# Kernel optimization log

Measured on AMD Instinct MI355X. Metric: run time of the kernel, lower is better.

Reference implementation:

```python
import jax, jax.numpy as jnp
import numpy as np

B = 4096          # batch of users
HIST = 200        # interacted items per user (padded/fixed)
NNEG = 20         # negatives per user
M_ITEM = 100000
DIM = 64
ALPHA = 0.5
BATA = 1e-4
LAMDA = 1e-4


def setup_inputs() -> dict:
    key = jax.random.key(0)
    k1, k2, k3, k4, k5, k6 = jax.random.split(key, 6)
    pos_items = jax.random.randint(k1, (B,), 0, M_ITEM)
    neg_items = jax.random.randint(k2, (B, NNEG), 0, M_ITEM)
    interacted_items = jax.random.randint(k3, (B, HIST), 0, M_ITEM)
    # per-user interaction counts (positive floats; original does num ** -alpha)
    user_item_num = jax.random.randint(k4, (B,), 1, 201).astype(jnp.float32)
    pu = jax.random.normal(k5, (M_ITEM, DIM), dtype=jnp.float32) * 0.001
    qi = jax.random.normal(k6, (M_ITEM, DIM), dtype=jnp.float32) * 0.001
    bi = jnp.zeros((M_ITEM, 1), dtype=jnp.float32)
    return {
        "pos_items": pos_items,
        "neg_items": neg_items,
        "user_item_num": user_item_num,
        "interacted_items": interacted_items,
        "pu": pu,
        "qi": qi,
        "bi": bi,
    }


def reference(pos_items, neg_items, user_item_num, interacted_items, pu, qi, bi):
    # EmbeddingBag-style ragged gather-sum: user embedding = sum of pu rows
    # of the user's interacted items. [B, HIST, DIM] -> [B, DIM]
    user_embeds = jnp.sum(pu[interacted_items], axis=1)

    b_i_i = bi[pos_items]            # [B, 1]
    b_i_j = bi[neg_items]            # [B, NNEG, 1]
    pos_embeds = qi[pos_items]       # [B, DIM]
    neg_embeds = qi[neg_items]       # [B, NNEG, DIM]

    t = user_item_num ** (-ALPHA)    # [B]

    # diag(user @ pos^T) == rowwise dot product
    pos_scores = t * jnp.sum(user_embeds * pos_embeds, axis=1) + b_i_i.T          # [1, B]
    neg_dot = jnp.einsum("bd,bnd->bn", user_embeds, neg_embeds)                    # [B, NNEG]
    neg_scores = t * neg_dot.T + b_i_j[:, :, 0].T                                  # [NNEG, B]

    # MSELoss(reduction='sum')(ones, pos - neg)
    diff = 1.0 - (pos_scores - neg_scores)                                         # [NNEG, B]
    loss = jnp.sum(diff ** 2)
    loss = loss \
        + BATA * jnp.sum(user_embeds ** 2) \
        + BATA * (jnp.sum(pos_embeds ** 2) + jnp.sum(neg_embeds ** 2)) \
        + LAMDA * (jnp.sum(b_i_i ** 2) + jnp.sum(b_i_j ** 2))
    return loss
```

## Files before the change

### kernel.cpp

```cpp
#include <hip/hip_runtime.h>

#define NB 4096
#define HIST 200
#define NNEG 20
#define DIM 64
#define BATA 1e-4f
#define LAMDA 1e-4f

__global__ __launch_bounds__(256) void fism_kernel(
    const int* __restrict__ pos_items,
    const int* __restrict__ neg_items,
    const float* __restrict__ user_item_num,
    const int* __restrict__ interacted,
    const float* __restrict__ pu,
    const float* __restrict__ qi,
    const float* __restrict__ bi,
    float* __restrict__ partials)
{
    const int wave = threadIdx.x >> 6;
    const int lane = threadIdx.x & 63;
    const int g    = lane >> 4;
    const int c    = lane & 15;
    const int gid  = wave * 4 + g;
    const int b    = blockIdx.x;

    __shared__ float4 s_u[4][16];
    __shared__ float  s_dot[24];
    __shared__ float  s_qsq[24];

    const float4* pu4 = (const float4*)pu;
    const float4* qi4 = (const float4*)qi;
    const int*    it  = interacted + b * HIST;
    const int*    negp = neg_items + b * NNEG;

    const int posi = pos_items[b];

    const int4* it4 = (const int4*)(it + gid * 12);
    int4 i0 = it4[0], i1 = it4[1], i2 = it4[2];
    int  tidx = it[192 + (gid & 7)];

    const int item0 = (gid == 0) ? posi : negp[gid - 1];
    float4 q0 = qi4[item0 * (DIM / 4) + c];
    float4 q1 = make_float4(0.f, 0.f, 0.f, 0.f);
    if (gid < 5) {
        int item1 = negp[gid + 15];
        q1 = qi4[item1 * (DIM / 4) + c];
    }

    float t_pow = 0.f, bp = 0.f, bn = 0.f;
    if (wave == 0) {
        t_pow = user_item_num[b];
        bp = bi[posi];
        if (lane < NNEG) bn = bi[negp[lane]];
    }

    float4 a0 = make_float4(0.f, 0.f, 0.f, 0.f);
    float4 a1 = make_float4(0.f, 0.f, 0.f, 0.f);
    {
        float4 v0  = pu4[i0.x * (DIM / 4) + c];
        float4 v1  = pu4[i0.y * (DIM / 4) + c];
        float4 v2  = pu4[i0.z * (DIM / 4) + c];
        float4 v3  = pu4[i0.w * (DIM / 4) + c];
        float4 v4  = pu4[i1.x * (DIM / 4) + c];
        float4 v5  = pu4[i1.y * (DIM / 4) + c];
        float4 v6  = pu4[i1.z * (DIM / 4) + c];
        float4 v7  = pu4[i1.w * (DIM / 4) + c];
        float4 v8  = pu4[i2.x * (DIM / 4) + c];
        float4 v9  = pu4[i2.y * (DIM / 4) + c];
        float4 v10 = pu4[i2.z * (DIM / 4) + c];
        float4 v11 = pu4[i2.w * (DIM / 4) + c];
        float4 vt  = pu4[tidx * (DIM / 4) + c];

        a0.x += v0.x + v1.x; a0.y += v0.y + v1.y; a0.z += v0.z + v1.z; a0.w += v0.w + v1.w;
        a1.x += v2.x + v3.x; a1.y += v2.y + v3.y; a1.z += v2.z + v3.z; a1.w += v2.w + v3.w;
        a0.x += v4.x + v5.x; a0.y += v4.y + v5.y; a0.z += v4.z + v5.z; a0.w += v4.w + v5.w;
        a1.x += v6.x + v7.x; a1.y += v6.y + v7.y; a1.z += v6.z + v7.z; a1.w += v6.w + v7.w;
        a0.x += v8.x + v9.x; a0.y += v8.y + v9.y; a0.z += v8.z + v9.z; a0.w += v8.w + v9.w;
        a1.x += v10.x + v11.x; a1.y += v10.y + v11.y; a1.z += v10.z + v11.z; a1.w += v10.w + v11.w;
        if (gid < 8) {
            a0.x += vt.x; a0.y += vt.y; a0.z += vt.z; a0.w += vt.w;
        }
    }
    float4 u = make_float4(a0.x + a1.x, a0.y + a1.y, a0.z + a1.z, a0.w + a1.w);

    #pragma unroll
    for (int m = 16; m <= 32; m <<= 1) {
        u.x += __shfl_xor(u.x, m);
        u.y += __shfl_xor(u.y, m);
        u.z += __shfl_xor(u.z, m);
        u.w += __shfl_xor(u.w, m);
    }
    if (lane < 16) s_u[wave][lane] = u;
    __syncthreads();

    float4 u0 = s_u[0][c], u1 = s_u[1][c], u2 = s_u[2][c], u3 = s_u[3][c];
    float4 ut = make_float4(u0.x + u1.x + u2.x + u3.x,
                            u0.y + u1.y + u2.y + u3.y,
                            u0.z + u1.z + u2.z + u3.z,
                            u0.w + u1.w + u2.w + u3.w);

    float contrib = 0.f;
    if (wave == 0 && g == 0)
        contrib += BATA * (ut.x*ut.x + ut.y*ut.y + ut.z*ut.z + ut.w*ut.w);

    {
        float dp = ut.x*q0.x + ut.y*q0.y + ut.z*q0.z + ut.w*q0.w;
        float qs = q0.x*q0.x + q0.y*q0.y + q0.z*q0.z + q0.w*q0.w;
        #pragma unroll
        for (int m = 1; m <= 8; m <<= 1) {
            dp += __shfl_xor(dp, m);
            qs += __shfl_xor(qs, m);
        }
        if (c == 0) { s_dot[gid] = dp; s_qsq[gid] = qs; }
    }
    if (gid < 5) {
        float dp = ut.x*q1.x + ut.y*q1.y + ut.z*q1.z + ut.w*q1.w;
        float qs = q1.x*q1.x + q1.y*q1.y + q1.z*q1.z + q1.w*q1.w;
        #pragma unroll
        for (int m = 1; m <= 8; m <<= 1) {
            dp += __shfl_xor(dp, m);
            qs += __shfl_xor(qs, m);
        }
        if (c == 0) { s_dot[gid + 16] = dp; s_qsq[gid + 16] = qs; }
    }
    __syncthreads();

    if (wave == 0) {
        const float t = 1.0f / sqrtf(t_pow);
        const float pos_score = t * s_dot[0] + bp;

        if (lane < NNEG) {
            float neg_score = t * s_dot[lane + 1] + bn;
            float d = 1.0f - pos_score + neg_score;
            contrib += d * d + LAMDA * bn * bn + BATA * s_qsq[lane + 1];
        }
        if (lane == 0)
            contrib += LAMDA * bp * bp + BATA * s_qsq[0];

        #pragma unroll
        for (int m = 1; m < 64; m <<= 1)
            contrib += __shfl_xor(contrib, m);
        if (lane == 0)
            partials[b] = contrib;
    }
}

__global__ __launch_bounds__(1024) void reduce_kernel(
    const float* __restrict__ part, float* __restrict__ out)
{
    __shared__ float s[16];
    const int t = threadIdx.x;
    float v = 0.f;
    #pragma unroll
    for (int k = 0; k < NB / 1024; ++k)
        v += part[t + k * 1024];
    #pragma unroll
    for (int m = 1; m < 64; m <<= 1)
        v += __shfl_xor(v, m);
    if ((t & 63) == 0) s[t >> 6] = v;
    __syncthreads();
    if (t < 16) {
        float x = s[t];
        #pragma unroll
        for (int m = 1; m < 16; m <<= 1)
            x += __shfl_xor(x, m);
        if (t == 0) out[0] = x;
    }
}

extern "C" void kernel_launch(void* const* d_in, const int* in_sizes, int n_in,
                              void* d_out, int out_size, void* d_ws, size_t ws_size,
                              hipStream_t stream) {
    const int*   pos_items     = (const int*)  d_in[0];
    const int*   neg_items     = (const int*)  d_in[1];
    const float* user_item_num = (const float*)d_in[2];
    const int*   interacted    = (const int*)  d_in[3];
    const float* pu            = (const float*)d_in[4];
    const float* qi            = (const float*)d_in[5];
    const float* bi            = (const float*)d_in[6];
    float* partials = (float*)d_ws;
    float* out = (float*)d_out;

    fism_kernel<<<NB, 256, 0, stream>>>(
        pos_items, neg_items, user_item_num, interacted, pu, qi, bi, partials);
    reduce_kernel<<<1, 1024, 0, stream>>>(partials, out);
}
```

Measured before the change: 38.48 us.

## Process eight users per block and reduce via atomicAdd instead of second kernel

Each block now loops over eight users, accumulating its loss locally and adding it to the output with a single atomicAdd. The output is zeroed with a memset, replacing the separate reduction kernel. This aims to cut per-block overhead and the second kernel launch. In exchange the grid shrinks, leaving fewer memory gathers in flight per CU, and users within a block are processed serially with barriers between them. Float atomics also make the summation order nondeterministic.

```diff
diff --git a/kernel.cpp b/kernel.cpp
--- a/kernel.cpp
+++ b/kernel.cpp
@@ -1,6 +1,8 @@
 #include <hip/hip_runtime.h>
 
 #define NB 4096
+#define UPB 8
+#define NBLK (NB / UPB)
 #define HIST 200
 #define NNEG 20
 #define DIM 64
@@ -15,14 +17,13 @@
     const float* __restrict__ pu,
     const float* __restrict__ qi,
     const float* __restrict__ bi,
-    float* __restrict__ partials)
+    float* __restrict__ out)
 {
     const int wave = threadIdx.x >> 6;
     const int lane = threadIdx.x & 63;
     const int g    = lane >> 4;
     const int c    = lane & 15;
     const int gid  = wave * 4 + g;
-    const int b    = blockIdx.x;
 
     __shared__ float4 s_u[4][16];
     __shared__ float  s_dot[24];
@@ -30,142 +31,127 @@
 
     const float4* pu4 = (const float4*)pu;
     const float4* qi4 = (const float4*)qi;
-    const int*    it  = interacted + b * HIST;
-    const int*    negp = neg_items + b * NNEG;
 
-    const int posi = pos_items[b];
+    float blockAcc = 0.f;
 
-    const int4* it4 = (const int4*)(it + gid * 12);
-    int4 i0 = it4[0], i1 = it4[1], i2 = it4[2];
-    int  tidx = it[192 + (gid & 7)];
+    for (int uu = 0; uu < UPB; ++uu) {
+        const int b = blockIdx.x * UPB + uu;
+        const int* it   = interacted + b * HIST;
+        const int* negp = neg_items + b * NNEG;
 
-    const int item0 = (gid == 0) ? posi : negp[gid - 1];
-    float4 q0 = qi4[item0 * (DIM / 4) + c];
-    float4 q1 = make_float4(0.f, 0.f, 0.f, 0.f);
-    if (gid < 5) {
-        int item1 = negp[gid + 15];
-        q1 = qi4[item1 * (DIM / 4) + c];
+        const int posi = pos_items[b];
+
+        const int4* it4 = (const int4*)(it + gid * 12);
+        int4 i0 = it4[0], i1 = it4[1], i2 = it4[2];
+        int  tidx = it[192 + (gid & 7)];
+
+        const int item0 = (gid == 0) ? posi : negp[gid - 1];
+        float4 q0 = qi4[item0 * (DIM / 4) + c];
+        float4 q1 = make_float4(0.f, 0.f, 0.f, 0.f);
+        if (gid < 5) {
+            int item1 = negp[gid + 15];
+            q1 = qi4[item1 * (DIM / 4) + c];
+        }
+
+        float t_pow = 0.f, bp = 0.f, bn = 0.f;
+        if (wave == 0) {
+            t_pow = user_item_num[b];
+            bp = bi[posi];
+            if (lane < NNEG) bn = bi[negp[lane]];
+        }
+
+        float4 a0 = make_float4(0.f, 0.f, 0.f, 0.f);
+        float4 a1 = make_float4(0.f, 0.f, 0.f, 0.f);
+        {
+            float4 v0  = pu4[i0.x * (DIM / 4) + c];
+            float4 v1  = pu4[i0.y * (DIM / 4) + c];
+            float4 v2  = pu4[i0.z * (DIM / 4) + c];
+            float4 v3  = pu4[i0.w * (DIM / 4) + c];
+            float4 v4  = pu4[i1.x * (DIM / 4) + c];
+            float4 v5  = pu4[i1.y * (DIM / 4) + c];
+            float4 v6  = pu4[i1.z * (DIM / 4) + c];
+            float4 v7  = pu4[i1.w * (DIM / 4) + c];
+            float4 v8  = pu4[i2.x * (DIM / 4) + c];
+            float4 v9  = pu4[i2.y * (DIM / 4) + c];
+            float4 v10 = pu4[i2.z * (DIM / 4) + c];
+            float4 v11 = pu4[i2.w * (DIM / 4) + c];
+            float4 vt  = pu4[tidx * (DIM / 4) + c];
+
+            a0.x += v0.x + v1.x; a0.y += v0.y + v1.y; a0.z += v0.z + v1.z; a0.w += v0.w + v1.w;
+            a1.x += v2.x + v3.x; a1.y += v2.y + v3.y; a1.z += v2.z + v3.z; a1.w += v2.w + v3.w;
+            a0.x += v4.x + v5.x; a0.y += v4.y + v5.y; a0.z += v4.z + v5.z; a0.w += v4.w + v5.w;
+            a1.x += v6.x + v7.x; a1.y += v6.y + v7.y; a1.z += v6.z + v7.z; a1.w += v6.w + v7.w;
+            a0.x += v8.x + v9.x; a0.y += v8.y + v9.y; a0.z += v8.z + v9.z; a0.w += v8.w + v9.w;
+            a1.x += v10.x + v11.x; a1.y += v10.y + v11.y; a1.z += v10.z + v11.z; a1.w += v10.w + v11.w;
+            if (gid < 8) {
+                a0.x += vt.x; a0.y += vt.y; a0.z += vt.z; a0.w += vt.w;
+            }
+        }
+        float4 u = make_float4(a0.x + a1.x, a0.y + a1.y, a0.z + a1.z, a0.w + a1.w);
+
+        #pragma unroll
+        for (int m = 16; m <= 32; m <<= 1) {
+            u.x += __shfl_xor(u.x, m);
+            u.y += __shfl_xor(u.y, m);
+            u.z += __shfl_xor(u.z, m);
+            u.w += __shfl_xor(u.w, m);
+        }
+        if (lane < 16) s_u[wave][lane] = u;
+        __syncthreads();
+
+        float4 u0 = s_u[0][c], u1 = s_u[1][c], u2 = s_u[2][c], u3 = s_u[3][c];
+        float4 ut = make_float4(u0.x + u1.x + u2.x + u3.x,
+                                u0.y + u1.y + u2.y + u3.y,
+                                u0.z + u1.z + u2.z + u3.z,
+                                u0.w + u1.w + u2.w + u3.w);
+
+        float contrib = 0.f;
+        if (wave == 0 && g == 0)
+            contrib += BATA * (ut.x*ut.x + ut.y*ut.y + ut.z*ut.z + ut.w*ut.w);
+
+        {
+            float dp = ut.x*q0.x + ut.y*q0.y + ut.z*q0.z + ut.w*q0.w;
+            float qs = q0.x*q0.x + q0.y*q0.y + q0.z*q0.z + q0.w*q0.w;
+            #pragma unroll
+            for (int m = 1; m <= 8; m <<= 1) {
+                dp += __shfl_xor(dp, m);
+                qs += __shfl_xor(qs, m);
+            }
+            if (c == 0) { s_dot[gid] = dp; s_qsq[gid] = qs; }
+        }
+        if (gid < 5) {
+            float dp = ut.x*q1.x + ut.y*q1.y + ut.z*q1.z + ut.w*q1.w;
+            float qs = q1.x*q1.x + q1.y*q1.y + q1.z*q1.z + q1.w*q1.w;
+            #pragma unroll
+            for (int m = 1; m <= 8; m <<= 1) {
+                dp += __shfl_xor(dp, m);
+                qs += __shfl_xor(qs, m);
+            }
+            if (c == 0) { s_dot[gid + 16] = dp; s_qsq[gid + 16] = qs; }
+        }
+        __syncthreads();
+
+        if (wave == 0) {
+            const float t = 1.0f / sqrtf(t_pow);
+            const float pos_score = t * s_dot[0] + bp;
+
+            if (lane < NNEG) {
+                float neg_score = t * s_dot[lane + 1] + bn;
+                float d = 1.0f - pos_score + neg_score;
+                contrib += d * d + LAMDA * bn * bn + BATA * s_qsq[lane + 1];
+            }
+            if (lane == 0)
+                contrib += LAMDA * bp * bp + BATA * s_qsq[0];
+
+            #pragma unroll
+            for (int m = 1; m < 64; m <<= 1)
+                contrib += __shfl_xor(contrib, m);
+            blockAcc += contrib;
+        }
     }
 
-    float t_pow = 0.f, bp = 0.f, bn = 0.f;
-    if (wave == 0) {
-        t_pow = user_item_num[b];
-        bp = bi[posi];
-        if (lane < NNEG) bn = bi[negp[lane]];
-    }
-
-    float4 a0 = make_float4(0.f, 0.f, 0.f, 0.f);
-    float4 a1 = make_float4(0.f, 0.f, 0.f, 0.f);
-    {
-        float4 v0  = pu4[i0.x * (DIM / 4) + c];
-        float4 v1  = pu4[i0.y * (DIM / 4) + c];
-        float4 v2  = pu4[i0.z * (DIM / 4) + c];
-        float4 v3  = pu4[i0.w * (DIM / 4) + c];
-        float4 v4  = pu4[i1.x * (DIM / 4) + c];
-        float4 v5  = pu4[i1.y * (DIM / 4) + c];
-        float4 v6  = pu4[i1.z * (DIM / 4) + c];
-        float4 v7  = pu4[i1.w * (DIM / 4) + c];
-        float4 v8  = pu4[i2.x * (DIM / 4) + c];
-        float4 v9  = pu4[i2.y * (DIM / 4) + c];
-        float4 v10 = pu4[i2.z * (DIM / 4) + c];
-        float4 v11 = pu4[i2.w * (DIM / 4) + c];
-        float4 vt  = pu4[tidx * (DIM / 4) + c];
-
-        a0.x += v0.x + v1.x; a0.y += v0.y + v1.y; a0.z += v0.z + v1.z; a0.w += v0.w + v1.w;
-        a1.x += v2.x + v3.x; a1.y += v2.y + v3.y; a1.z += v2.z + v3.z; a1.w += v2.w + v3.w;
-        a0.x += v4.x + v5.x; a0.y += v4.y + v5.y; a0.z += v4.z + v5.z; a0.w += v4.w + v5.w;
-        a1.x += v6.x + v7.x; a1.y += v6.y + v7.y; a1.z += v6.z + v7.z; a1.w += v6.w + v7.w;
-        a0.x += v8.x + v9.x; a0.y += v8.y + v9.y; a0.z += v8.z + v9.z; a0.w += v8.w + v9.w;
-        a1.x += v10.x + v11.x; a1.y += v10.y + v11.y; a1.z += v10.z + v11.z; a1.w += v10.w + v11.w;
-        if (gid < 8) {
-            a0.x += vt.x; a0.y += vt.y; a0.z += vt.z; a0.w += vt.w;
-        }
-    }
-    float4 u = make_float4(a0.x + a1.x, a0.y + a1.y, a0.z + a1.z, a0.w + a1.w);
-
-    #pragma unroll
-    for (int m = 16; m <= 32; m <<= 1) {
-        u.x += __shfl_xor(u.x, m);
-        u.y += __shfl_xor(u.y, m);
-        u.z += __shfl_xor(u.z, m);
-        u.w += __shfl_xor(u.w, m);
-    }
-    if (lane < 16) s_u[wave][lane] = u;
-    __syncthreads();
-
-    float4 u0 = s_u[0][c], u1 = s_u[1][c], u2 = s_u[2][c], u3 = s_u[3][c];
-    float4 ut = make_float4(u0.x + u1.x + u2.x + u3.x,
-                            u0.y + u1.y + u2.y + u3.y,
-                            u0.z + u1.z + u2.z + u3.z,
-                            u0.w + u1.w + u2.w + u3.w);
-
-    float contrib = 0.f;
-    if (wave == 0 && g == 0)
-        contrib += BATA * (ut.x*ut.x + ut.y*ut.y + ut.z*ut.z + ut.w*ut.w);
-
-    {
-        float dp = ut.x*q0.x + ut.y*q0.y + ut.z*q0.z + ut.w*q0.w;
-        float qs = q0.x*q0.x + q0.y*q0.y + q0.z*q0.z + q0.w*q0.w;
-        #pragma unroll
-        for (int m = 1; m <= 8; m <<= 1) {
-            dp += __shfl_xor(dp, m);
-            qs += __shfl_xor(qs, m);
-        }
-        if (c == 0) { s_dot[gid] = dp; s_qsq[gid] = qs; }
-    }
-    if (gid < 5) {
-        float dp = ut.x*q1.x + ut.y*q1.y + ut.z*q1.z + ut.w*q1.w;
-        float qs = q1.x*q1.x + q1.y*q1.y + q1.z*q1.z + q1.w*q1.w;
-        #pragma unroll
-        for (int m = 1; m <= 8; m <<= 1) {
-            dp += __shfl_xor(dp, m);
-            qs += __shfl_xor(qs, m);
-        }
-        if (c == 0) { s_dot[gid + 16] = dp; s_qsq[gid + 16] = qs; }
-    }
-    __syncthreads();
-
-    if (wave == 0) {
-        const float t = 1.0f / sqrtf(t_pow);
-        const float pos_score = t * s_dot[0] + bp;
-
-        if (lane < NNEG) {
-            float neg_score = t * s_dot[lane + 1] + bn;
-            float d = 1.0f - pos_score + neg_score;
-            contrib += d * d + LAMDA * bn * bn + BATA * s_qsq[lane + 1];
-        }
-        if (lane == 0)
-            contrib += LAMDA * bp * bp + BATA * s_qsq[0];
-
-        #pragma unroll
-        for (int m = 1; m < 64; m <<= 1)
-            contrib += __shfl_xor(contrib, m);
-        if (lane == 0)
-            partials[b] = contrib;
-    }
-}
-
-__global__ __launch_bounds__(1024) void reduce_kernel(
-    const float* __restrict__ part, float* __restrict__ out)
-{
-    __shared__ float s[16];
-    const int t = threadIdx.x;
-    float v = 0.f;
-    #pragma unroll
-    for (int k = 0; k < NB / 1024; ++k)
-        v += part[t + k * 1024];
-    #pragma unroll
-    for (int m = 1; m < 64; m <<= 1)
-        v += __shfl_xor(v, m);
-    if ((t & 63) == 0) s[t >> 6] = v;
-    __syncthreads();
-    if (t < 16) {
-        float x = s[t];
-        #pragma unroll
-        for (int m = 1; m < 16; m <<= 1)
-            x += __shfl_xor(x, m);
-        if (t == 0) out[0] = x;
-    }
+    if (wave == 0 && lane == 0)
+        atomicAdd(out, blockAcc);
 }
 
 extern "C" void kernel_launch(void* const* d_in, const int* in_sizes, int n_in,
@@ -178,10 +164,9 @@
     const float* pu            = (const float*)d_in[4];
     const float* qi            = (const float*)d_in[5];
     const float* bi            = (const float*)d_in[6];
-    float* partials = (float*)d_ws;
     float* out = (float*)d_out;
 
-    fism_kernel<<<NB, 256, 0, stream>>>(
-        pos_items, neg_items, user_item_num, interacted, pu, qi, bi, partials);
-    reduce_kernel<<<1, 1024, 0, stream>>>(partials, out);
+    hipMemsetAsync(out, 0, sizeof(float), stream);
+    fism_kernel<<<NBLK, 256, 0, stream>>>(
+        pos_items, neg_items, user_item_num, interacted, pu, qi, bi, out);
 }
```

Result: slower. 48.78 us (+26.8%).

## Fuse final reduction into main kernel via bucketed atomics and last-block-wins

Applied to the files above, without the earlier changes.

Removes the separate reduce kernel launch. Each block atomically adds its partial into one of 64 cache-line-spaced buckets, bumps a per-bucket counter, and the last finisher across all buckets sums the buckets and writes the output. A hipMemsetAsync is added to zero the workspace each call, which trades one kernel launch for a memset and introduces atomic contention and nondeterministic float summation order.

```diff
diff --git a/kernel.cpp b/kernel.cpp
--- a/kernel.cpp
+++ b/kernel.cpp
@@ -7,6 +7,11 @@
 #define BATA 1e-4f
 #define LAMDA 1e-4f
 
+#define NBUCKET 64
+#define WS_SUB_OFF   4096
+#define WS_SUPER_OFF 8192
+#define WS_ZERO_BYTES 8256
+
 __global__ __launch_bounds__(256) void fism_kernel(
     const int* __restrict__ pos_items,
     const int* __restrict__ neg_items,
@@ -15,7 +20,8 @@
     const float* __restrict__ pu,
     const float* __restrict__ qi,
     const float* __restrict__ bi,
-    float* __restrict__ partials)
+    char* __restrict__ ws,
+    float* __restrict__ out)
 {
     const int wave = threadIdx.x >> 6;
     const int lane = threadIdx.x & 63;
@@ -27,6 +33,7 @@
     __shared__ float4 s_u[4][16];
     __shared__ float  s_dot[24];
     __shared__ float  s_qsq[24];
+    __shared__ int    s_won;
 
     const float4* pu4 = (const float4*)pu;
     const float4* qi4 = (const float4*)qi;
@@ -140,31 +147,30 @@
         #pragma unroll
         for (int m = 1; m < 64; m <<= 1)
             contrib += __shfl_xor(contrib, m);
+
+        if (lane == 0) {
+            const int bk = b & (NBUCKET - 1);
+            atomicAdd((float*)(ws + bk * 64), contrib);
+            asm volatile("s_waitcnt vmcnt(0)" ::: "memory");
+            unsigned old = atomicAdd((unsigned*)(ws + WS_SUB_OFF + bk * 64), 1u);
+            int won = 0;
+            if (old == (NB / NBUCKET) - 1) {
+                unsigned so = atomicAdd((unsigned*)(ws + WS_SUPER_OFF), 1u);
+                won = (so == NBUCKET - 1);
+            }
+            s_won = won;
+        }
+    }
+    __syncthreads();
+
+    if (s_won && wave == 0) {
+        float v = __hip_atomic_load((const float*)(ws + lane * 64),
+                                    __ATOMIC_RELAXED, __HIP_MEMORY_SCOPE_AGENT);
+        #pragma unroll
+        for (int m = 1; m < 64; m <<= 1)
+            v += __shfl_xor(v, m);
         if (lane == 0)
-            partials[b] = contrib;
-    }
-}
-
-__global__ __launch_bounds__(1024) void reduce_kernel(
-    const float* __restrict__ part, float* __restrict__ out)
-{
-    __shared__ float s[16];
-    const int t = threadIdx.x;
-    float v = 0.f;
-    #pragma unroll
-    for (int k = 0; k < NB / 1024; ++k)
-        v += part[t + k * 1024];
-    #pragma unroll
-    for (int m = 1; m < 64; m <<= 1)
-        v += __shfl_xor(v, m);
-    if ((t & 63) == 0) s[t >> 6] = v;
-    __syncthreads();
-    if (t < 16) {
-        float x = s[t];
-        #pragma unroll
-        for (int m = 1; m < 16; m <<= 1)
-            x += __shfl_xor(x, m);
-        if (t == 0) out[0] = x;
+            out[0] = v;
     }
 }
 
@@ -178,10 +184,10 @@
     const float* pu            = (const float*)d_in[4];
     const float* qi            = (const float*)d_in[5];
     const float* bi            = (const float*)d_in[6];
-    float* partials = (float*)d_ws;
+    char*  ws  = (char*)d_ws;
     float* out = (float*)d_out;
 
+    hipMemsetAsync(ws, 0, WS_ZERO_BYTES, stream);
     fism_kernel<<<NB, 256, 0, stream>>>(
-        pos_items, neg_items, user_item_num, interacted, pu, qi, bi, partials);
-    reduce_kernel<<<1, 1024, 0, stream>>>(partials, out);
+        pos_items, neg_items, user_item_num, interacted, pu, qi, bi, ws, out);
 }
```

Measured after the change: 43.91 us. +14.1%, slower.
